# Performance work log

Hardware: AMD Instinct MI355X
Metric: run time of the kernel (lower is better)

The kernel has to match this reference:

```python
import jax, jax.numpy as jnp
import numpy as np

NUM_HEADS = 16
CAUSAL = True


def setup_inputs() -> dict:
    key = jax.random.key(0)
    ks = jax.random.split(key, 3)
    B, T, D = 2, 2048, 1024
    s = 1.0 / np.sqrt(D)
    return {
        "x": jax.random.normal(ks[0], (B, T, D), dtype=jnp.float32),
        "W_qkv": jax.random.normal(ks[1], (3 * D, D), dtype=jnp.float32) * s,
        "b_qkv": jnp.zeros((3 * D,), dtype=jnp.float32),
        "W_out": jax.random.normal(ks[2], (D, D), dtype=jnp.float32) * s,
        "b_out": jnp.zeros((D,), dtype=jnp.float32),
    }


def reference(x, W_qkv, b_qkv, W_out, b_out):
    B, T, D = x.shape
    H = NUM_HEADS
    hd = D // H
    # qkv projection: torch Linear y = x @ W.T + b
    qkv = jnp.einsum('btd,ed->bte', x, W_qkv) + b_qkv  # [B,T,3D]
    qkv = qkv.reshape(B, T, H, 3 * hd).transpose(0, 2, 1, 3)  # [B,H,T,3hd]
    q, k, v = jnp.split(qkv, 3, axis=-1)  # each [B,H,T,hd]
    scale = 1.0 / np.sqrt(hd).astype(np.float32)
    scores = jnp.einsum('bhtd,bhsd->bhts', q, k) * scale  # [B,H,T,T]
    if CAUSAL:
        mask = jnp.triu(jnp.ones((T, T), dtype=bool), k=1)
        scores = jnp.where(mask, jnp.float32(-jnp.inf), scores)
    weights = jax.nn.softmax(scores, axis=-1)
    attn = jnp.einsum('bhts,bhsd->bhtd', weights, v)  # [B,H,T,hd]
    out = attn.transpose(0, 2, 1, 3).reshape(B, T, D)
    return jnp.einsum('btd,ed->bte', out, W_out) + b_out
```

## Files before the change

### kernel.cpp

```cpp
#include <hip/hip_runtime.h>
#include <hip/hip_bf16.h>
#include <cstdint>


using short8  = __attribute__((ext_vector_type(8))) short;
using floatx4 = __attribute__((ext_vector_type(4))) float;

#define LDS_STRIDE 40

__device__ __forceinline__ float bf16_to_f32(unsigned short u) {
    union { unsigned int i; float f; } v; v.i = ((unsigned int)u) << 16; return v.f;
}
__device__ __forceinline__ unsigned short f32_to_bf16(float f) {
    union { float f; unsigned int i; } v; v.f = f;
    unsigned int x = v.i;
    unsigned int r = x + 0x7FFFu + ((x >> 16) & 1u);
    return (unsigned short)(r >> 16);
}
__device__ __forceinline__ short8 cvt8(const float* __restrict__ p) {
    const float4 f0 = *(const float4*)p;
    const float4 f1 = *(const float4*)(p + 4);
    short8 r;
    r[0] = (short)f32_to_bf16(f0.x); r[1] = (short)f32_to_bf16(f0.y);
    r[2] = (short)f32_to_bf16(f0.z); r[3] = (short)f32_to_bf16(f0.w);
    r[4] = (short)f32_to_bf16(f1.x); r[5] = (short)f32_to_bf16(f1.y);
    r[6] = (short)f32_to_bf16(f1.z); r[7] = (short)f32_to_bf16(f1.w);
    return r;
}
__device__ __forceinline__ unsigned int cvtpk(float a, float b) {
    unsigned int r;
    asm("v_cvt_pk_bf16_f32 %0, %1, %2" : "=v"(r) : "v"(a), "v"(b));
    return r;
}

#define Q_PRESCALE 0.1803368801111204f

#if __has_builtin(__builtin_amdgcn_global_load_lds)
#define ASYNC_STAGE 1
typedef const __attribute__((address_space(1))) void* gas1_t;
typedef __attribute__((address_space(3))) void* las3_t;
#else
#define ASYNC_STAGE 0
#endif

__device__ __forceinline__ void gload_lds16(const ushort* g, ushort* l) {
#if ASYNC_STAGE
    __builtin_amdgcn_global_load_lds((gas1_t)g, (las3_t)l, 16, 0, 0);
#else
    *(short8*)l = *(const short8*)g;
#endif
}

__device__ __forceinline__ int v_slot(int k) {
    const int k5 = k & 31;
    return (k & 32) + ((k5 >> 4) & 1) * 4 + ((k5 >> 2) & 3) * 8 + (k5 & 3);
}

__global__ __launch_bounds__(256, 8) void cvt_bf16_3(
    const float* __restrict__ x,  const float* __restrict__ wq,
    const float* __restrict__ wo, ushort* __restrict__ xb,
    ushort* __restrict__ wqb, ushort* __restrict__ wob)
{
    const int i = blockIdx.x * 256 + threadIdx.x;
    const float* src; ushort* dst; int off;
    if (i < 524288)      { src = x;  dst = xb;  off = i; }
    else if (i < 917504) { src = wq; dst = wqb; off = i - 524288; }
    else                 { src = wo; dst = wob; off = i - 917504; }
    *(short8*)(dst + (size_t)off * 8) = cvt8(src + (size_t)off * 8);
}

template <int MODE>
__global__ __launch_bounds__(256, 3) void gemm_bf16(
    const ushort* __restrict__ A, const ushort* __restrict__ W,
    const float* __restrict__ bias,
    ushort* __restrict__ Cq, ushort* __restrict__ Ck, ushort* __restrict__ Cv,
    float* __restrict__ Cout, int M, int N, int K)
{
    __shared__ __align__(16) ushort As[2][128 * 32];
    __shared__ __align__(16) ushort Bs[2][128 * 32];

    const int tid  = threadIdx.x;
    const int lane = tid & 63;
    const int wave = tid >> 6;
    const int wm = (wave >> 1) * 64;
    const int wn = (wave & 1) * 64;
    const int m0 = blockIdx.x * 128;
    const int n0 = blockIdx.y * 128;
    const int quad = lane >> 4;
    const int l16  = lane & 15;

    floatx4 acc[4][4];
#pragma unroll
    for (int i = 0; i < 4; i++)
#pragma unroll
        for (int j = 0; j < 4; j++) acc[i][j] = (floatx4)0.0f;

    const int ob0 = tid * 16, ob1 = ob0 + 4096;
    const int ln0 = ob0 >> 7, p0_ = ((ob0 >> 4) & 7) ^ (ln0 & 7);
    const int ln1 = ob1 >> 7, p1_ = ((ob1 >> 4) & 7) ^ (ln1 & 7);
    const int row0 = ln0 * 2 + (p0_ >> 2), ch0 = p0_ & 3;
    const int row1 = ln1 * 2 + (p1_ >> 2), ch1 = p1_ & 3;
    const ushort* pA0 = A + (size_t)(m0 + row0) * K + ch0 * 8;
    const ushort* pA1 = A + (size_t)(m0 + row1) * K + ch1 * 8;
    const ushort* pB0 = W + (size_t)(n0 + row0) * K + ch0 * 8;
    const ushort* pB1 = W + (size_t)(n0 + row1) * K + ch1 * 8;

    const int Ra = wm + l16;
    const int aoff = (Ra >> 1) * 64 + (((((Ra & 1) << 2) + quad) ^ ((Ra >> 1) & 7)) << 3);
    const int Rb = wn + l16;
    const int boff = (Rb >> 1) * 64 + (((((Rb & 1) << 2) + quad) ^ ((Rb >> 1) & 7)) << 3);

    auto stage = [&](int k0, ushort* AsB, ushort* BsB) {
        gload_lds16(pA0 + k0, AsB + wave * 512);
        gload_lds16(pA1 + k0, AsB + 2048 + wave * 512);
        gload_lds16(pB0 + k0, BsB + wave * 512);
        gload_lds16(pB1 + k0, BsB + 2048 + wave * 512);
    };
    auto compute = [&](const ushort* AsB, const ushort* BsB) {
        short8 af[4], bf[4];
#pragma unroll
        for (int i = 0; i < 4; i++)
            af[i] = *(const short8*)&AsB[aoff + i * 512];
#pragma unroll
        for (int j = 0; j < 4; j++)
            bf[j] = *(const short8*)&BsB[boff + j * 512];
#pragma unroll
        for (int i = 0; i < 4; i++)
#pragma unroll
            for (int j = 0; j < 4; j++)
                acc[i][j] = __builtin_amdgcn_mfma_f32_16x16x32_bf16(af[i], bf[j], acc[i][j], 0, 0, 0);
    };

#if ASYNC_STAGE
    stage(0, As[0], Bs[0]);
    __syncthreads();
    int k = 0;
    while (true) {
        if (k + 32 < K) stage(k + 32, As[1], Bs[1]);
        compute(As[0], Bs[0]);
        __syncthreads();
        k += 32; if (k >= K) break;
        if (k + 32 < K) stage(k + 32, As[0], Bs[0]);
        compute(As[1], Bs[1]);
        __syncthreads();
        k += 32; if (k >= K) break;
    }
#else
    for (int k0 = 0; k0 < K; k0 += 32) {
        const short8 a0 = *(const short8*)(pA0 + k0);
        const short8 a1 = *(const short8*)(pA1 + k0);
        const short8 b0 = *(const short8*)(pB0 + k0);
        const short8 b1 = *(const short8*)(pB1 + k0);
        __syncthreads();
        *(short8*)((char*)As[0] + ob0) = a0;
        *(short8*)((char*)As[0] + ob1) = a1;
        *(short8*)((char*)Bs[0] + ob0) = b0;
        *(short8*)((char*)Bs[0] + ob1) = b1;
        __syncthreads();
        compute(As[0], Bs[0]);
    }
#endif

#pragma unroll
    for (int i = 0; i < 4; i++) {
#pragma unroll
        for (int j = 0; j < 4; j++) {
#pragma unroll
            for (int r = 0; r < 4; r++) {
                const int row = m0 + wm + i * 16 + quad * 4 + r;
                const int col = n0 + wn + j * 16 + l16;
                float v = acc[i][j][r] + bias[col];
                if (MODE == 0) {
                    const int h  = col / 192;
                    const int rr = col - h * 192;
                    const int sel = rr >> 6;
                    const int d   = rr & 63;
                    const int b = row >> 11;
                    const int t = row & 2047;
                    const int bh = b * 16 + h;
                    if (sel == 0) {
                        Cq[(((size_t)bh) * 2048 + t) * 64 + d] =
                            f32_to_bf16(v * Q_PRESCALE);
                    } else if (sel == 1) {
                        Ck[(((size_t)bh) * 2048 + t) * 64 + d] = f32_to_bf16(v);
                    } else {
                        Cv[(((size_t)bh * 32 + (t >> 6)) * 64 + d) * 64 + v_slot(t & 63)] =
                            f32_to_bf16(v);
                    }
                } else {
                    Cout[(size_t)row * N + col] = v;
                }
            }
        }
    }
}

template <int MODE, int AFP32>
__global__ __launch_bounds__(256, 2) void gemm_bt(
    const void* __restrict__ Av, const float* __restrict__ W,
    const float* __restrict__ bias,
    ushort* __restrict__ Cq, ushort* __restrict__ Ck, ushort* __restrict__ Cv,
    float* __restrict__ Cout, int M, int N, int K)
{
    __shared__ __align__(16) ushort As[128 * LDS_STRIDE];
    __shared__ __align__(16) ushort Bs[128 * LDS_STRIDE];

    const int tid  = threadIdx.x;
    const int lane = tid & 63;
    const int wave = tid >> 6;
    const int wm = (wave >> 1) * 64;
    const int wn = (wave & 1) * 64;
    const int m0 = blockIdx.x * 128;
    const int n0 = blockIdx.y * 128;
    const int quad = lane >> 4;
    const int l16  = lane & 15;

    floatx4 acc[4][4];
#pragma unroll
    for (int i = 0; i < 4; i++)
#pragma unroll
        for (int j = 0; j < 4; j++) acc[i][j] = (floatx4)0.0f;

    const int srow = tid >> 2;
    const int scol = (tid & 3) * 8;

    for (int k0 = 0; k0 < K; k0 += 32) {
        short8 a0, a1;
        if (AFP32) {
            const float* A = (const float*)Av;
            a0 = cvt8(A + (size_t)(m0 + srow) * K + k0 + scol);
            a1 = cvt8(A + (size_t)(m0 + srow + 64) * K + k0 + scol);
        } else {
            const ushort* A = (const ushort*)Av;
            a0 = *(const short8*)(A + (size_t)(m0 + srow) * K + k0 + scol);
            a1 = *(const short8*)(A + (size_t)(m0 + srow + 64) * K + k0 + scol);
        }
        const short8 b0 = cvt8(W + (size_t)(n0 + srow) * K + k0 + scol);
        const short8 b1 = cvt8(W + (size_t)(n0 + srow + 64) * K + k0 + scol);
        __syncthreads();
        *(short8*)&As[srow * LDS_STRIDE + scol] = a0;
        *(short8*)&As[(srow + 64) * LDS_STRIDE + scol] = a1;
        *(short8*)&Bs[srow * LDS_STRIDE + scol] = b0;
        *(short8*)&Bs[(srow + 64) * LDS_STRIDE + scol] = b1;
        __syncthreads();

        short8 af[4], bf[4];
#pragma unroll
        for (int i = 0; i < 4; i++)
            af[i] = *(const short8*)&As[(wm + i * 16 + l16) * LDS_STRIDE + quad * 8];
#pragma unroll
        for (int j = 0; j < 4; j++)
            bf[j] = *(const short8*)&Bs[(wn + j * 16 + l16) * LDS_STRIDE + quad * 8];
#pragma unroll
        for (int i = 0; i < 4; i++)
#pragma unroll
            for (int j = 0; j < 4; j++)
                acc[i][j] = __builtin_amdgcn_mfma_f32_16x16x32_bf16(af[i], bf[j], acc[i][j], 0, 0, 0);
    }

#pragma unroll
    for (int i = 0; i < 4; i++) {
#pragma unroll
        for (int j = 0; j < 4; j++) {
#pragma unroll
            for (int r = 0; r < 4; r++) {
                const int row = m0 + wm + i * 16 + quad * 4 + r;
                const int col = n0 + wn + j * 16 + l16;
                float v = acc[i][j][r] + bias[col];
                if (MODE == 0) {
                    const int h  = col / 192;
                    const int rr = col - h * 192;
                    const int sel = rr >> 6;
                    const int d   = rr & 63;
                    const int b = row >> 11;
                    const int t = row & 2047;
                    const int bh = b * 16 + h;
                    if (sel == 0) {
                        Cq[(((size_t)bh) * 2048 + t) * 64 + d] =
                            f32_to_bf16(v * Q_PRESCALE);
                    } else if (sel == 1) {
                        Ck[(((size_t)bh) * 2048 + t) * 64 + d] = f32_to_bf16(v);
                    } else {
                        Cv[(((size_t)bh * 32 + (t >> 6)) * 64 + d) * 64 + v_slot(t & 63)] =
                            f32_to_bf16(v);
                    }
                } else {
                    Cout[(size_t)row * N + col] = v;
                }
            }
        }
    }
}

__global__ __launch_bounds__(256, 2) void attn_mfma(
    const ushort* __restrict__ Q, const ushort* __restrict__ K,
    const ushort* __restrict__ Vtb, ushort* __restrict__ O)
{
    const int bid   = blockIdx.x;
    const int bh    = bid & 31;
    const int qtIdx = bid >> 5;
    const int qt    = (qtIdx < 8) ? (15 - qtIdx) : (qtIdx - 8);
    const int tid  = threadIdx.x;
    const int wave = tid >> 6;
    const int lane = tid & 63;
    const int quad = lane >> 4;
    const int l16  = lane & 15;
    const int qb   = qt * 128 + wave * 32;

    __shared__ __align__(16) ushort Ks[2][8192];
    __shared__ __align__(16) ushort Vs[2][8192];

    const size_t kbase = (size_t)bh * 2048 * 64;

    int e[4];
#pragma unroll
    for (int c = 0; c < 4; c++) {
        const int ob  = tid * 16 + c * 4096;
        const int sub = ob >> 13;
        const int obs = ob & 8191;
        const int r   = obs >> 7;
        const int ch  = (obs >> 4) & 7;
        e[c] = sub * 4096 + r * 64 + ((ch ^ (r & 7)) << 3);
    }
    const ushort* Kb = K + kbase;
    const ushort* Vb = Vtb + (size_t)bh * 32 * 4096;

    auto stage = [&](int t128, ushort* KsB, ushort* VsB) {
        const ushort* Ktile = Kb + t128 * 8192;
        const ushort* Vtile = Vb + t128 * 8192;
#pragma unroll
        for (int c = 0; c < 4; c++)
            gload_lds16(Ktile + e[c], KsB + c * 2048 + wave * 512);
#pragma unroll
        for (int c = 0; c < 4; c++)
            gload_lds16(Vtile + e[c], VsB + c * 2048 + wave * 512);
    };

    const int sw0 = ((quad ^ (l16 & 7)) << 3);
    const int sw1 = (((4 + quad) ^ (l16 & 7)) << 3);
    const int rbase = l16 * 64;

    short8 qf0[2], qf1[2];
#pragma unroll
    for (int f = 0; f < 2; f++) {
        const ushort* qp = Q + kbase + (size_t)(qb + f * 16 + l16) * 64 + quad * 8;
        qf0[f] = *(const short8*)qp;
        qf1[f] = *(const short8*)(qp + 32);
    }

    floatx4 accO[2][4];
#pragma unroll
    for (int f = 0; f < 2; f++)
#pragma unroll
        for (int d = 0; d < 4; d++) accO[f][d] = (floatx4)0.0f;
    float accLs[2] = {0.0f, 0.0f};

    union PB { unsigned int u[4]; short8 s8; };

    auto compute = [&](int t128, const ushort* KsB, const ushort* VsB) {
#pragma unroll
        for (int s = 0; s < 2; ++s) {
            const int t64 = 2 * t128 + s;
            if (t64 * 64 > qb + 31) continue;
            const ushort* Kt = KsB + s * 4096;
            const ushort* Vt = VsB + s * 4096;
            short8 kf[4][2], vf[4][2];
#pragma unroll
            for (int j = 0; j < 4; j++) {
                kf[j][0] = *(const short8*)&Kt[j * 1024 + rbase + sw0];
                kf[j][1] = *(const short8*)&Kt[j * 1024 + rbase + sw1];
            }
#pragma unroll
            for (int d = 0; d < 4; d++) {
                vf[d][0] = *(const short8*)&Vt[d * 1024 + rbase + sw0];
                vf[d][1] = *(const short8*)&Vt[d * 1024 + rbase + sw1];
            }

#pragma unroll
            for (int f = 0; f < 2; f++) {
                const int qlo = qb + f * 16;
                if (t64 * 64 > qlo + 15) continue;
                floatx4 sc[4];
#pragma unroll
                for (int j = 0; j < 4; j++) {
                    floatx4 acc = (floatx4)0.0f;
                    acc = __builtin_amdgcn_mfma_f32_16x16x32_bf16(kf[j][0], qf0[f], acc, 0, 0, 0);
                    acc = __builtin_amdgcn_mfma_f32_16x16x32_bf16(kf[j][1], qf1[f], acc, 0, 0, 0);
                    sc[j] = acc;
                }
                if (t64 * 64 + 63 > qlo) {
                    const int qcol = qlo + l16;
#pragma unroll
                    for (int j = 0; j < 4; j++) {
                        const int keyb = t64 * 64 + j * 16 + quad * 4;
#pragma unroll
                        for (int r = 0; r < 4; r++)
                            if (keyb + r > qcol) sc[j][r] = -1e30f;
                    }
                }
#pragma unroll
                for (int j = 0; j < 4; j++)
#pragma unroll
                    for (int r = 0; r < 4; r++)
                        sc[j][r] = __builtin_amdgcn_exp2f(sc[j][r]);
                const floatx4 ssum = sc[0] + sc[1] + sc[2] + sc[3];
                accLs[f] += (ssum[0] + ssum[1]) + (ssum[2] + ssum[3]);
                PB p0, p1;
#pragma unroll
                for (int j = 0; j < 2; j++) {
                    p0.u[j * 2 + 0] = cvtpk(sc[j][0], sc[j][1]);
                    p0.u[j * 2 + 1] = cvtpk(sc[j][2], sc[j][3]);
                    p1.u[j * 2 + 0] = cvtpk(sc[j + 2][0], sc[j + 2][1]);
                    p1.u[j * 2 + 1] = cvtpk(sc[j + 2][2], sc[j + 2][3]);
                }
#pragma unroll
                for (int d = 0; d < 4; d++) {
                    accO[f][d] = __builtin_amdgcn_mfma_f32_16x16x32_bf16(p0.s8, vf[d][0], accO[f][d], 0, 0, 0);
                    accO[f][d] = __builtin_amdgcn_mfma_f32_16x16x32_bf16(p1.s8, vf[d][1], accO[f][d], 0, 0, 0);
                }
            }
        }
    };

    const int nt = qt + 1;
    stage(0, Ks[0], Vs[0]);
    __syncthreads();
    int t = 0;
    while (true) {
        if (t + 1 < nt) stage(t + 1, Ks[1], Vs[1]);
        compute(t, Ks[0], Vs[0]);
        __syncthreads();
        if (++t >= nt) break;
        if (t + 1 < nt) stage(t + 1, Ks[0], Vs[0]);
        compute(t, Ks[1], Vs[1]);
        __syncthreads();
        if (++t >= nt) break;
    }

    const int b = bh >> 4, h = bh & 15;
#pragma unroll
    for (int f = 0; f < 2; f++) {
        float L = accLs[f];
        L += __shfl_xor(L, 16);
        L += __shfl_xor(L, 32);
        float inv[4];
#pragma unroll
        for (int r = 0; r < 4; r++) inv[r] = 1.0f / __shfl(L, quad * 4 + r);
#pragma unroll
        for (int d = 0; d < 4; d++)
#pragma unroll
            for (int r = 0; r < 4; r++)
                O[(size_t)(b * 2048 + qb + f * 16 + quad * 4 + r) * 1024 + h * 64 + d * 16 + l16] =
                    f32_to_bf16(accO[f][d][r] * inv[r]);
    }
}

extern "C" void kernel_launch(void* const* d_in, const int* in_sizes, int n_in,
                              void* d_out, int out_size, void* d_ws, size_t ws_size,
                              hipStream_t stream) {
    const float* x    = (const float*)d_in[0];
    const float* Wqkv = (const float*)d_in[1];
    const float* bqkv = (const float*)d_in[2];
    const float* Wout = (const float*)d_in[3];
    const float* bout = (const float*)d_in[4];
    float* out = (float*)d_out;

    char* ws = (char*)d_ws;
    const size_t MB = 1024 * 1024;
    ushort* Q    = (ushort*)(ws + 0 * MB);
    ushort* Kk   = (ushort*)(ws + 8 * MB);
    ushort* Vtb  = (ushort*)(ws + 16 * MB);
    ushort* O    = (ushort*)(ws + 24 * MB);

    const dim3 blk(256);
    if (ws_size >= 48 * MB) {
        ushort* xb    = (ushort*)(ws + 32 * MB);
        ushort* Wqkvb = (ushort*)(ws + 40 * MB);
        ushort* Woutb = (ushort*)(ws + 46 * MB);
        cvt_bf16_3<<<dim3(4096), blk, 0, stream>>>(x, Wqkv, Wout, xb, Wqkvb, Woutb);
        gemm_bf16<0><<<dim3(32, 24), blk, 0, stream>>>(xb, Wqkvb, bqkv, Q, Kk, Vtb,
                                                       nullptr, 4096, 3072, 1024);
        attn_mfma<<<dim3(512), blk, 0, stream>>>(Q, Kk, Vtb, O);
        gemm_bf16<1><<<dim3(32, 8), blk, 0, stream>>>(O, Woutb, bout, nullptr, nullptr,
                                                      nullptr, out, 4096, 1024, 1024);
    } else {
        gemm_bt<0, 1><<<dim3(32, 24), blk, 0, stream>>>(x, Wqkv, bqkv, Q, Kk, Vtb,
                                                        nullptr, 4096, 3072, 1024);
        attn_mfma<<<dim3(512), blk, 0, stream>>>(Q, Kk, Vtb, O);
        gemm_bt<1, 0><<<dim3(32, 8), blk, 0, stream>>>(O, Wout, bout, nullptr, nullptr,
                                                       nullptr, out, 4096, 1024, 1024);
    }
}
```

Baseline: 170.3 us.

## Halve attention query tile to 64 rows and key tile to 64, doubling grid

The attention kernel now handles 64 query rows per block (16 per wave) instead of 128, stages 64-key K/V tiles instead of 128, and launches 1024 blocks with a launch bound of 4 blocks per CU instead of 2. This raises occupancy and parallelism and gives finer causal load balancing, which is meant to cut tail imbalance and idle CUs. V fragment loads now happen after softmax, which lowers register pressure. In exchange, each staged K/V tile is reused by fewer query rows, so LDS and global traffic per FLOP rises and there are more barriers per unit of work.

```diff
diff --git a/kernel.cpp b/kernel.cpp
--- a/kernel.cpp
+++ b/kernel.cpp
@@ -292,137 +292,115 @@
     }
 }
 
-__global__ __launch_bounds__(256, 2) void attn_mfma(
+__global__ __launch_bounds__(256, 4) void attn_mfma(
     const ushort* __restrict__ Q, const ushort* __restrict__ K,
     const ushort* __restrict__ Vtb, ushort* __restrict__ O)
 {
     const int bid   = blockIdx.x;
     const int bh    = bid & 31;
     const int qtIdx = bid >> 5;
-    const int qt    = (qtIdx < 8) ? (15 - qtIdx) : (qtIdx - 8);
+    const int qi    = (qtIdx < 16) ? (31 - qtIdx) : (qtIdx - 16);
     const int tid  = threadIdx.x;
     const int wave = tid >> 6;
     const int lane = tid & 63;
     const int quad = lane >> 4;
     const int l16  = lane & 15;
-    const int qb   = qt * 128 + wave * 32;
-
-    __shared__ __align__(16) ushort Ks[2][8192];
-    __shared__ __align__(16) ushort Vs[2][8192];
+    const int qb   = qi * 64 + wave * 16;
+
+    __shared__ __align__(16) ushort Ks[2][4096];
+    __shared__ __align__(16) ushort Vs[2][4096];
 
     const size_t kbase = (size_t)bh * 2048 * 64;
 
-    int e[4];
-#pragma unroll
-    for (int c = 0; c < 4; c++) {
-        const int ob  = tid * 16 + c * 4096;
-        const int sub = ob >> 13;
-        const int obs = ob & 8191;
-        const int r   = obs >> 7;
-        const int ch  = (obs >> 4) & 7;
-        e[c] = sub * 4096 + r * 64 + ((ch ^ (r & 7)) << 3);
-    }
+    const int ob0 = tid * 16, ob1 = ob0 + 4096;
+    const int r0 = ob0 >> 7, c0 = (ob0 >> 4) & 7;
+    const int r1 = ob1 >> 7, c1 = (ob1 >> 4) & 7;
+    const int e0 = r0 * 64 + ((c0 ^ (r0 & 7)) << 3);
+    const int e1 = r1 * 64 + ((c1 ^ (r1 & 7)) << 3);
     const ushort* Kb = K + kbase;
     const ushort* Vb = Vtb + (size_t)bh * 32 * 4096;
 
-    auto stage = [&](int t128, ushort* KsB, ushort* VsB) {
-        const ushort* Ktile = Kb + t128 * 8192;
-        const ushort* Vtile = Vb + t128 * 8192;
-#pragma unroll
-        for (int c = 0; c < 4; c++)
-            gload_lds16(Ktile + e[c], KsB + c * 2048 + wave * 512);
-#pragma unroll
-        for (int c = 0; c < 4; c++)
-            gload_lds16(Vtile + e[c], VsB + c * 2048 + wave * 512);
+    auto stage = [&](int t, ushort* KsB, ushort* VsB) {
+        const ushort* Ktile = Kb + t * 4096;
+        const ushort* Vtile = Vb + t * 4096;
+        gload_lds16(Ktile + e0, KsB + wave * 512);
+        gload_lds16(Ktile + e1, KsB + 2048 + wave * 512);
+        gload_lds16(Vtile + e0, VsB + wave * 512);
+        gload_lds16(Vtile + e1, VsB + 2048 + wave * 512);
     };
 
     const int sw0 = ((quad ^ (l16 & 7)) << 3);
     const int sw1 = (((4 + quad) ^ (l16 & 7)) << 3);
     const int rbase = l16 * 64;
 
-    short8 qf0[2], qf1[2];
-#pragma unroll
-    for (int f = 0; f < 2; f++) {
-        const ushort* qp = Q + kbase + (size_t)(qb + f * 16 + l16) * 64 + quad * 8;
-        qf0[f] = *(const short8*)qp;
-        qf1[f] = *(const short8*)(qp + 32);
-    }
-
-    floatx4 accO[2][4];
-#pragma unroll
-    for (int f = 0; f < 2; f++)
-#pragma unroll
-        for (int d = 0; d < 4; d++) accO[f][d] = (floatx4)0.0f;
-    float accLs[2] = {0.0f, 0.0f};
+    short8 qf0, qf1;
+    {
+        const ushort* qp = Q + kbase + (size_t)(qb + l16) * 64 + quad * 8;
+        qf0 = *(const short8*)qp;
+        qf1 = *(const short8*)(qp + 32);
+    }
+
+    floatx4 accO[4];
+#pragma unroll
+    for (int d = 0; d < 4; d++) accO[d] = (floatx4)0.0f;
+    float accLs = 0.0f;
 
     union PB { unsigned int u[4]; short8 s8; };
 
-    auto compute = [&](int t128, const ushort* KsB, const ushort* VsB) {
-#pragma unroll
-        for (int s = 0; s < 2; ++s) {
-            const int t64 = 2 * t128 + s;
-            if (t64 * 64 > qb + 31) continue;
-            const ushort* Kt = KsB + s * 4096;
-            const ushort* Vt = VsB + s * 4096;
-            short8 kf[4][2], vf[4][2];
+    auto compute = [&](int t, const ushort* KsB, const ushort* VsB) {
+        short8 kf[4][2];
+#pragma unroll
+        for (int j = 0; j < 4; j++) {
+            kf[j][0] = *(const short8*)&KsB[j * 1024 + rbase + sw0];
+            kf[j][1] = *(const short8*)&KsB[j * 1024 + rbase + sw1];
+        }
+        floatx4 sc[4];
+#pragma unroll
+        for (int j = 0; j < 4; j++) {
+            floatx4 acc = (floatx4)0.0f;
+            acc = __builtin_amdgcn_mfma_f32_16x16x32_bf16(kf[j][0], qf0, acc, 0, 0, 0);
+            acc = __builtin_amdgcn_mfma_f32_16x16x32_bf16(kf[j][1], qf1, acc, 0, 0, 0);
+            sc[j] = acc;
+        }
+        if (t * 64 + 63 > qb) {
+            const int qcol = qb + l16;
 #pragma unroll
             for (int j = 0; j < 4; j++) {
-                kf[j][0] = *(const short8*)&Kt[j * 1024 + rbase + sw0];
-                kf[j][1] = *(const short8*)&Kt[j * 1024 + rbase + sw1];
+                const int keyb = t * 64 + j * 16 + quad * 4;
+#pragma unroll
+                for (int r = 0; r < 4; r++)
+                    if (keyb + r > qcol) sc[j][r] = -1e30f;
             }
-#pragma unroll
-            for (int d = 0; d < 4; d++) {
-                vf[d][0] = *(const short8*)&Vt[d * 1024 + rbase + sw0];
-                vf[d][1] = *(const short8*)&Vt[d * 1024 + rbase + sw1];
-            }
-
-#pragma unroll
-            for (int f = 0; f < 2; f++) {
-                const int qlo = qb + f * 16;
-                if (t64 * 64 > qlo + 15) continue;
-                floatx4 sc[4];
-#pragma unroll
-                for (int j = 0; j < 4; j++) {
-                    floatx4 acc = (floatx4)0.0f;
-                    acc = __builtin_amdgcn_mfma_f32_16x16x32_bf16(kf[j][0], qf0[f], acc, 0, 0, 0);
-                    acc = __builtin_amdgcn_mfma_f32_16x16x32_bf16(kf[j][1], qf1[f], acc, 0, 0, 0);
-                    sc[j] = acc;
-                }
-                if (t64 * 64 + 63 > qlo) {
-                    const int qcol = qlo + l16;
-#pragma unroll
-                    for (int j = 0; j < 4; j++) {
-                        const int keyb = t64 * 64 + j * 16 + quad * 4;
-#pragma unroll
-                        for (int r = 0; r < 4; r++)
-                            if (keyb + r > qcol) sc[j][r] = -1e30f;
-                    }
-                }
-#pragma unroll
-                for (int j = 0; j < 4; j++)
-#pragma unroll
-                    for (int r = 0; r < 4; r++)
-                        sc[j][r] = __builtin_amdgcn_exp2f(sc[j][r]);
-                const floatx4 ssum = sc[0] + sc[1] + sc[2] + sc[3];
-                accLs[f] += (ssum[0] + ssum[1]) + (ssum[2] + ssum[3]);
-                PB p0, p1;
-#pragma unroll
-                for (int j = 0; j < 2; j++) {
-                    p0.u[j * 2 + 0] = cvtpk(sc[j][0], sc[j][1]);
-                    p0.u[j * 2 + 1] = cvtpk(sc[j][2], sc[j][3]);
-                    p1.u[j * 2 + 0] = cvtpk(sc[j + 2][0], sc[j + 2][1]);
-                    p1.u[j * 2 + 1] = cvtpk(sc[j + 2][2], sc[j + 2][3]);
-                }
-#pragma unroll
-                for (int d = 0; d < 4; d++) {
-                    accO[f][d] = __builtin_amdgcn_mfma_f32_16x16x32_bf16(p0.s8, vf[d][0], accO[f][d], 0, 0, 0);
-                    accO[f][d] = __builtin_amdgcn_mfma_f32_16x16x32_bf16(p1.s8, vf[d][1], accO[f][d], 0, 0, 0);
-                }
-            }
+        }
+#pragma unroll
+        for (int j = 0; j < 4; j++)
+#pragma unroll
+            for (int r = 0; r < 4; r++)
+                sc[j][r] = __builtin_amdgcn_exp2f(sc[j][r]);
+        const floatx4 ssum = sc[0] + sc[1] + sc[2] + sc[3];
+        accLs += (ssum[0] + ssum[1]) + (ssum[2] + ssum[3]);
+        PB p0, p1;
+#pragma unroll
+        for (int j = 0; j < 2; j++) {
+            p0.u[j * 2 + 0] = cvtpk(sc[j][0], sc[j][1]);
+            p0.u[j * 2 + 1] = cvtpk(sc[j][2], sc[j][3]);
+            p1.u[j * 2 + 0] = cvtpk(sc[j + 2][0], sc[j + 2][1]);
+            p1.u[j * 2 + 1] = cvtpk(sc[j + 2][2], sc[j + 2][3]);
+        }
+        short8 vf[4][2];
+#pragma unroll
+        for (int d = 0; d < 4; d++) {
+            vf[d][0] = *(const short8*)&VsB[d * 1024 + rbase + sw0];
+            vf[d][1] = *(const short8*)&VsB[d * 1024 + rbase + sw1];
+        }
+#pragma unroll
+        for (int d = 0; d < 4; d++) {
+            accO[d] = __builtin_amdgcn_mfma_f32_16x16x32_bf16(p0.s8, vf[d][0], accO[d], 0, 0, 0);
+            accO[d] = __builtin_amdgcn_mfma_f32_16x16x32_bf16(p1.s8, vf[d][1], accO[d], 0, 0, 0);
         }
     };
 
-    const int nt = qt + 1;
+    const int nt = qi + 1;
     stage(0, Ks[0], Vs[0]);
     __syncthreads();
     int t = 0;
@@ -438,9 +416,8 @@
     }
 
     const int b = bh >> 4, h = bh & 15;
-#pragma unroll
-    for (int f = 0; f < 2; f++) {
-        float L = accLs[f];
+    {
+        float L = accLs;
         L += __shfl_xor(L, 16);
         L += __shfl_xor(L, 32);
         float inv[4];
@@ -450,8 +427,8 @@
         for (int d = 0; d < 4; d++)
 #pragma unroll
             for (int r = 0; r < 4; r++)
-                O[(size_t)(b * 2048 + qb + f * 16 + quad * 4 + r) * 1024 + h * 64 + d * 16 + l16] =
-                    f32_to_bf16(accO[f][d][r] * inv[r]);
+                O[(size_t)(b * 2048 + qb + quad * 4 + r) * 1024 + h * 64 + d * 16 + l16] =
+                    f32_to_bf16(accO[d][r] * inv[r]);
     }
 }
 
@@ -480,13 +457,13 @@
         cvt_bf16_3<<<dim3(4096), blk, 0, stream>>>(x, Wqkv, Wout, xb, Wqkvb, Woutb);
         gemm_bf16<0><<<dim3(32, 24), blk, 0, stream>>>(xb, Wqkvb, bqkv, Q, Kk, Vtb,
                                                        nullptr, 4096, 3072, 1024);
-        attn_mfma<<<dim3(512), blk, 0, stream>>>(Q, Kk, Vtb, O);
+        attn_mfma<<<dim3(1024), blk, 0, stream>>>(Q, Kk, Vtb, O);
         gemm_bf16<1><<<dim3(32, 8), blk, 0, stream>>>(O, Woutb, bout, nullptr, nullptr,
                                                       nullptr, out, 4096, 1024, 1024);
     } else {
         gemm_bt<0, 1><<<dim3(32, 24), blk, 0, stream>>>(x, Wqkv, bqkv, Q, Kk, Vtb,
                                                         nullptr, 4096, 3072, 1024);
-        attn_mfma<<<dim3(512), blk, 0, stream>>>(Q, Kk, Vtb, O);
+        attn_mfma<<<dim3(1024), blk, 0, stream>>>(Q, Kk, Vtb, O);
         gemm_bt<1, 0><<<dim3(32, 8), blk, 0, stream>>>(O, Wout, bout, nullptr, nullptr,
                                                        nullptr, out, 4096, 1024, 1024);
     }
```

New measurement: 170.3 us. About the same (-0.0%).
